# Optimization experiments

Measured on AMD Instinct MI355X. Metric: run time of the kernel, lower is better.

## Reference

```python
import jax, jax.numpy as jnp
import numpy as np

N_HEADS = 16
EMBD = 1024
D_HEAD = EMBD // N_HEADS

def setup_inputs() -> dict:
    key = jax.random.key(0)
    ks = jax.random.split(key, 5)
    x = jax.random.normal(ks[0], (2, 2048, EMBD), dtype=jnp.float32)
    # Linear weights stored torch-style [out, in]; apply as x @ W.T + b
    W_in = jax.random.normal(ks[1], (3 * EMBD, EMBD), dtype=jnp.float32) * (EMBD ** -0.5)
    b_in = jax.random.normal(ks[2], (3 * EMBD,), dtype=jnp.float32) * 0.01
    W_out = jax.random.normal(ks[3], (EMBD, EMBD), dtype=jnp.float32) * (EMBD ** -0.5)
    b_out = jax.random.normal(ks[4], (EMBD,), dtype=jnp.float32) * 0.01
    return {"x": x, "W_in": W_in, "b_in": b_in, "W_out": W_out, "b_out": b_out}

def reference(x, W_in, b_in, W_out, b_out):
    B, S, D = x.shape
    qkv = x @ W_in.T + b_in                      # [B, S, 3D]
    q, k, v = jnp.split(qkv, 3, axis=-1)
    def heads(t):
        return t.reshape(B, S, N_HEADS, D_HEAD).transpose(0, 2, 1, 3)  # [B,H,S,d]
    q, k, v = heads(q), heads(k), heads(v)
    scale = 1.0 / jnp.sqrt(jnp.float32(D_HEAD))
    scores = jnp.einsum('bhqd,bhkd->bhqk', q, k) * scale
    weights = jax.nn.softmax(scores, axis=-1)
    out = jnp.einsum('bhqk,bhkd->bhqd', weights, v)  # [B,H,S,d]
    out = out.transpose(0, 2, 1, 3).reshape(B, S, D)
    return out @ W_out.T + b_out
```

## Files before the change

kernel.cpp:

```cpp
#include <hip/hip_runtime.h>
#include <cstdint>

#define EMBD 1024
#define NH 16
#define DH 64
#define BB 2
#define SS 2048
#define M_TOT (BB*SS)
#define N_QKV (3*EMBD)

typedef __bf16 bf16_t;
typedef bf16_t bf16x8 __attribute__((ext_vector_type(8)));
typedef float f32x4 __attribute__((ext_vector_type(4)));
typedef unsigned short u16;
typedef unsigned int u32;

static __device__ __forceinline__ u16 f2bf(float f) {
    union { float f; unsigned u; } c; c.f = f;
    unsigned u = c.u;
    unsigned r = (u + 0x7FFFu + ((u >> 16) & 1u)) >> 16;
    return (u16)r;
}

#define GLDS16(gp, lp) \
    __builtin_amdgcn_global_load_lds((const __attribute__((address_space(1))) void*)(gp), \
                                     (__attribute__((address_space(3))) void*)(lp), 16, 0, 0)

#define NX8 (M_TOT * EMBD / 8)
#define NWI8 (N_QKV * EMBD / 8)
#define NWO8 (EMBD * EMBD / 8)
__global__ void cast_all(const float* __restrict__ x, const float* __restrict__ wi,
                         const float* __restrict__ wo, u16* __restrict__ xb,
                         u16* __restrict__ wib, u16* __restrict__ wob) {
    int i = blockIdx.x * blockDim.x + threadIdx.x;
    const float* s; u16* d; int off;
    if (i < NX8)              { s = x;  d = xb;  off = i; }
    else if (i < NX8 + NWI8)  { s = wi; d = wib; off = i - NX8; }
    else                      { s = wo; d = wob; off = i - NX8 - NWI8; }
    const float4* s4 = (const float4*)s;
    float4 a = s4[2 * off];
    float4 b = s4[2 * off + 1];
    union { u16 u[8]; uint4 v; } r;
    r.u[0] = f2bf(a.x); r.u[1] = f2bf(a.y); r.u[2] = f2bf(a.z); r.u[3] = f2bf(a.w);
    r.u[4] = f2bf(b.x); r.u[5] = f2bf(b.y); r.u[6] = f2bf(b.z); r.u[7] = f2bf(b.w);
    ((uint4*)d)[off] = r.v;
}

#define QSCALE (0.125f * 1.4426950408889634f)
__global__ __launch_bounds__(256) void gemm_qkv(
    const u16* __restrict__ Xb,
    const u16* __restrict__ Wb,
    const float* __restrict__ b_in,
    u16* __restrict__ Q, u16* __restrict__ Kf, u16* __restrict__ Vpf)
{
    __shared__ u16 AB[3][8192];
    const int t = threadIdx.x;
    const int lane = t & 63;
    const int wave = t >> 6;
    const int wm = wave >> 1, wn = wave & 1;
    const int quad = lane >> 4, l16 = lane & 15;
    const int m0 = blockIdx.y * 128, n0 = blockIdx.x * 128;

    const int s0i = t, s1i = 256 + t;
    const u16* ga0 = Xb + (size_t)(m0 + (s0i >> 2)) * EMBD + (s0i & 3) * 8;
    const u16* ga1 = Xb + (size_t)(m0 + (s1i >> 2)) * EMBD + (s1i & 3) * 8;
    const u16* gb0 = Wb + (size_t)(n0 + (s0i >> 2)) * EMBD + (s0i & 3) * 8;
    const u16* gb1 = Wb + (size_t)(n0 + (s1i >> 2)) * EMBD + (s1i & 3) * 8;

    f32x4 acc[4][4] = {};

#pragma unroll
    for (int p = 0; p < 2; ++p) {
        u16* buf = &AB[p][0];
        GLDS16(ga0 + p * 32, buf + s0i * 8);
        GLDS16(ga1 + p * 32, buf + s1i * 8);
        GLDS16(gb0 + p * 32, buf + 4096 + s0i * 8);
        GLDS16(gb1 + p * 32, buf + 4096 + s1i * 8);
    }

    int bi = 0;
    int bw = 2;
    for (int it = 0; it < EMBD / 32; ++it) {
        asm volatile("s_waitcnt vmcnt(4)" ::: "memory");
        __syncthreads();
        {
            int k0 = (it + 2) * 32;
            u16* buf = &AB[bw][0];
            GLDS16(ga0 + k0, buf + s0i * 8);
            GLDS16(ga1 + k0, buf + s1i * 8);
            GLDS16(gb0 + k0, buf + 4096 + s0i * 8);
            GLDS16(gb1 + k0, buf + 4096 + s1i * 8);
        }
        const u16* As = &AB[bi][0];
        const u16* Bs = &AB[bi][4096];
        bf16x8 af[4], bfr[4];
#pragma unroll
        for (int im = 0; im < 4; ++im)
            af[im] = *(const bf16x8*)(As + (wm * 64 + im * 16 + l16) * 32 + quad * 8);
#pragma unroll
        for (int in = 0; in < 4; ++in)
            bfr[in] = *(const bf16x8*)(Bs + (wn * 64 + in * 16 + l16) * 32 + quad * 8);
#pragma unroll
        for (int im = 0; im < 4; ++im)
#pragma unroll
            for (int in = 0; in < 4; ++in)
                acc[im][in] = __builtin_amdgcn_mfma_f32_16x16x32_bf16(
                    af[im], bfr[in], acc[im][in], 0, 0, 0);
        bi = (bi == 2) ? 0 : bi + 1;
        bw = (bw == 2) ? 0 : bw + 1;
    }

#pragma unroll
    for (int im = 0; im < 4; ++im) {
        int rbase = m0 + wm * 64 + im * 16 + quad * 4;
        int b = rbase >> 11, ss = rbase & (SS - 1);
#pragma unroll
        for (int in = 0; in < 4; ++in) {
            int col = n0 + wn * 64 + in * 16 + l16;
            float bias = b_in[col];
            float v0 = acc[im][in][0] + bias;
            float v1 = acc[im][in][1] + bias;
            float v2 = acc[im][in][2] + bias;
            float v3 = acc[im][in][3] + bias;
            if (col < EMBD) {
                int h = col >> 6, d = col & 63;
                u16* qp = Q + (((size_t)(b * NH + h) * SS) + ss) * DH + d;
                qp[0]      = f2bf(v0 * QSCALE);
                qp[DH]     = f2bf(v1 * QSCALE);
                qp[2 * DH] = f2bf(v2 * QSCALE);
                qp[3 * DH] = f2bf(v3 * QSCALE);
            } else if (col < 2 * EMBD) {
                int c = col - EMBD; int h = c >> 6, d = c & 63;
                int qf = (d >> 3) & 3;
                int sA = (ss >> 1) & 3;
                int sB = (sA + 1) & 3;
                u16* kp = Kf + (size_t)(b * NH + h) * SS * DH
                          + (ss >> 4) * 1024 + (d >> 5) * 512
                          + (ss & 15) * 32 + (d & 7);
                kp[(qf ^ sA) * 8]      = f2bf(v0);
                kp[32 + (qf ^ sA) * 8] = f2bf(v1);
                kp[64 + (qf ^ sB) * 8] = f2bf(v2);
                kp[96 + (qf ^ sB) * 8] = f2bf(v3);
            } else {
                int c = col - 2 * EMBD; int h = c >> 6, d = c & 63;
                int p32 = ((((ss >> 2) & 3) ^ ((d >> 1) & 3)) * 8)
                          + ((ss >> 4) & 1) * 4;
                u32 lo = (u32)f2bf(v0) | ((u32)f2bf(v1) << 16);
                u32 hi = (u32)f2bf(v2) | ((u32)f2bf(v3) << 16);
                uint2 pk; pk.x = lo; pk.y = hi;
                *(uint2*)(Vpf + (size_t)(b * NH + h) * SS * DH
                          + (ss >> 5) * 2048 + (d >> 4) * 512 + (d & 15) * 32 + p32) = pk;
            }
        }
    }
}

#define OST 72
#define NCH (SS / 64)
__global__ __launch_bounds__(256, 2) void attn(
    const u16* __restrict__ Q, const u16* __restrict__ Kf,
    const u16* __restrict__ Vpf, u16* __restrict__ AO)
{
    __shared__ u16 KV[3][8192];
    const int t = threadIdx.x;
    const int lane = t & 63, w = t >> 6;
    const int quad = lane >> 4, l16 = lane & 15;
    const int sq8 = (quad ^ ((l16 >> 1) & 3)) * 8;
    const int b0 = blockIdx.x;
    const int bh = (b0 & 7) * 4 + ((b0 >> 3) & 3);
    const int qt = b0 >> 5;
    const int q0 = qt * 128 + w * 32;

    const u16* Qh = Q + ((size_t)bh * SS + q0) * DH;
    const u16* Kh = Kf + (size_t)bh * SS * DH;
    const u16* Vh = Vpf + (size_t)bh * SS * DH;

    bf16x8 qb[2][2];
#pragma unroll
    for (int qi = 0; qi < 2; ++qi) {
        qb[qi][0] = *(const bf16x8*)(Qh + (qi * 16 + l16) * DH + quad * 8);
        qb[qi][1] = *(const bf16x8*)(Qh + (qi * 16 + l16) * DH + 32 + quad * 8);
    }

    union { u16 u[8]; bf16x8 b; } onesu;
#pragma unroll
    for (int j = 0; j < 8; ++j) onesu.u[j] = 0x3F80u;
    const bf16x8 ones = onesu.b;

    f32x4 o[2][4] = {};
    f32x4 ol[2] = {};

#pragma unroll
    for (int p = 0; p < 2; ++p) {
        GLDS16(Kh + p * 4096 + t * 8,        &KV[p][0] + t * 8);
        GLDS16(Kh + p * 4096 + 2048 + t * 8, &KV[p][0] + 2048 + t * 8);
        GLDS16(Vh + p * 4096 + t * 8,        &KV[p][4096] + t * 8);
        GLDS16(Vh + p * 4096 + 2048 + t * 8, &KV[p][4096] + 2048 + t * 8);
    }

    int bi = 0, bw = 2;
    for (int it = 0; it < NCH; ++it) {
        asm volatile("s_waitcnt vmcnt(4)" ::: "memory");
        __syncthreads();
        if (it < NCH - 1) {
            const u16* kc = Kh + (it + 2) * 4096;
            const u16* vc = Vh + (it + 2) * 4096;
            u16* kb = &KV[bw][0];
            u16* vb = &KV[bw][4096];
            GLDS16(kc + t * 8,        kb + t * 8);
            GLDS16(kc + 2048 + t * 8, kb + 2048 + t * 8);
            GLDS16(vc + t * 8,        vb + t * 8);
            GLDS16(vc + 2048 + t * 8, vb + 2048 + t * 8);
        }
        const u16* Kb = &KV[bi][0];
        const u16* Vb = &KV[bi][4096];
#pragma unroll
        for (int g = 0; g < 2; ++g) {
            bf16x8 ka00 = *(const bf16x8*)(Kb + (2 * g) * 1024 +       l16 * 32 + sq8);
            bf16x8 ka01 = *(const bf16x8*)(Kb + (2 * g) * 1024 + 512 + l16 * 32 + sq8);
            bf16x8 ka10 = *(const bf16x8*)(Kb + (2 * g + 1) * 1024 +       l16 * 32 + sq8);
            bf16x8 ka11 = *(const bf16x8*)(Kb + (2 * g + 1) * 1024 + 512 + l16 * 32 + sq8);
            bf16x8 va0 = *(const bf16x8*)(Vb + g * 2048 +        l16 * 32 + sq8);
            bf16x8 va1 = *(const bf16x8*)(Vb + g * 2048 + 512  + l16 * 32 + sq8);
            bf16x8 va2 = *(const bf16x8*)(Vb + g * 2048 + 1024 + l16 * 32 + sq8);
            bf16x8 va3 = *(const bf16x8*)(Vb + g * 2048 + 1536 + l16 * 32 + sq8);
            bf16x8 pb[2];
#pragma unroll
            for (int qi = 0; qi < 2; ++qi) {
                f32x4 z0 = {0.f, 0.f, 0.f, 0.f};
                f32x4 z1 = {0.f, 0.f, 0.f, 0.f};
                __builtin_amdgcn_s_setprio(1);
                z0 = __builtin_amdgcn_mfma_f32_16x16x32_bf16(ka00, qb[qi][0], z0, 0, 0, 0);
                z0 = __builtin_amdgcn_mfma_f32_16x16x32_bf16(ka01, qb[qi][1], z0, 0, 0, 0);
                z1 = __builtin_amdgcn_mfma_f32_16x16x32_bf16(ka10, qb[qi][0], z1, 0, 0, 0);
                z1 = __builtin_amdgcn_mfma_f32_16x16x32_bf16(ka11, qb[qi][1], z1, 0, 0, 0);
                __builtin_amdgcn_s_setprio(0);
                u32 ue[8];
#pragma unroll
                for (int j = 0; j < 4; ++j) {
                    float e0 = __builtin_amdgcn_exp2f(z0[j]);
                    float e1 = __builtin_amdgcn_exp2f(z1[j]);
                    union { float f; u32 v; } c0, c1;
                    c0.f = e0; c1.f = e1;
                    ue[j] = c0.v + 0x8000u;
                    ue[4 + j] = c1.v + 0x8000u;
                }
                union { uint4 u; bf16x8 b; } cv;
                cv.u.x = __builtin_amdgcn_perm(ue[1], ue[0], 0x07060302u);
                cv.u.y = __builtin_amdgcn_perm(ue[3], ue[2], 0x07060302u);
                cv.u.z = __builtin_amdgcn_perm(ue[5], ue[4], 0x07060302u);
                cv.u.w = __builtin_amdgcn_perm(ue[7], ue[6], 0x07060302u);
                pb[qi] = cv.b;
            }
            __builtin_amdgcn_s_setprio(1);
            o[0][0] = __builtin_amdgcn_mfma_f32_16x16x32_bf16(va0, pb[0], o[0][0], 0, 0, 0);
            o[0][1] = __builtin_amdgcn_mfma_f32_16x16x32_bf16(va1, pb[0], o[0][1], 0, 0, 0);
            o[0][2] = __builtin_amdgcn_mfma_f32_16x16x32_bf16(va2, pb[0], o[0][2], 0, 0, 0);
            o[0][3] = __builtin_amdgcn_mfma_f32_16x16x32_bf16(va3, pb[0], o[0][3], 0, 0, 0);
            ol[0]   = __builtin_amdgcn_mfma_f32_16x16x32_bf16(ones, pb[0], ol[0], 0, 0, 0);
            o[1][0] = __builtin_amdgcn_mfma_f32_16x16x32_bf16(va0, pb[1], o[1][0], 0, 0, 0);
            o[1][1] = __builtin_amdgcn_mfma_f32_16x16x32_bf16(va1, pb[1], o[1][1], 0, 0, 0);
            o[1][2] = __builtin_amdgcn_mfma_f32_16x16x32_bf16(va2, pb[1], o[1][2], 0, 0, 0);
            o[1][3] = __builtin_amdgcn_mfma_f32_16x16x32_bf16(va3, pb[1], o[1][3], 0, 0, 0);
            ol[1]   = __builtin_amdgcn_mfma_f32_16x16x32_bf16(ones, pb[1], ol[1], 0, 0, 0);
            __builtin_amdgcn_s_setprio(0);
        }
        bi = (bi == 2) ? 0 : bi + 1;
        bw = (bw == 2) ? 0 : bw + 1;
    }

    float rl[2];
    rl[0] = 1.0f / ol[0][0];
    rl[1] = 1.0f / ol[1][0];
    __syncthreads();
    u16* Ksc = &KV[0][0];
#pragma unroll
    for (int qi = 0; qi < 2; ++qi)
#pragma unroll
        for (int dt = 0; dt < 4; ++dt)
#pragma unroll
            for (int jj = 0; jj < 2; ++jj) {
                u32 lo_ = (u32)f2bf(o[qi][dt][2 * jj] * rl[qi]);
                u32 hi_ = (u32)f2bf(o[qi][dt][2 * jj + 1] * rl[qi]);
                *(u32*)(Ksc + (w * 32 + qi * 16 + l16) * OST + dt * 16 + quad * 4 + jj * 2) =
                    lo_ | (hi_ << 16);
            }
    __syncthreads();
    const int b = bh >> 4, h = bh & 15;
#pragma unroll
    for (int i = 0; i < 4; ++i) {
        int idx = i * 256 + t;
        int q = idx >> 3, c = idx & 7;
        uint4 vv = *(const uint4*)(Ksc + q * OST + c * 8);
        *(uint4*)(AO + ((size_t)(b * SS + qt * 128 + q)) * EMBD + h * DH + c * 8) = vv;
    }
}

__global__ __launch_bounds__(256) void gemm_out(
    const u16* __restrict__ Ab,
    const u16* __restrict__ Wb,
    const float* __restrict__ b_out,
    float* __restrict__ Out)
{
    __shared__ u16 AB[3][6144];
    const int t = threadIdx.x;
    const int lane = t & 63;
    const int wave = t >> 6;
    const int quad = lane >> 4, l16 = lane & 15;
    const int m0 = blockIdx.y * 128, n0 = blockIdx.x * 64;

    const u16* ga0 = Ab + (size_t)(m0 + (t >> 2)) * EMBD + (t & 3) * 8;
    const u16* ga1 = Ab + (size_t)(m0 + 64 + (t >> 2)) * EMBD + (t & 3) * 8;
    const u16* gb0 = Wb + (size_t)(n0 + (t >> 2)) * EMBD + (t & 3) * 8;

    f32x4 acc[2][4] = {};

#pragma unroll
    for (int p = 0; p < 2; ++p) {
        u16* buf = &AB[p][0];
        GLDS16(ga0 + p * 32, buf + t * 8);
        GLDS16(ga1 + p * 32, buf + 2048 + t * 8);
        GLDS16(gb0 + p * 32, buf + 4096 + t * 8);
    }

    int bi = 0, bw = 2;
    for (int it = 0; it < EMBD / 32; ++it) {
        asm volatile("s_waitcnt vmcnt(3)" ::: "memory");
        __syncthreads();
        {
            int k0 = (it + 2) * 32;
            u16* buf = &AB[bw][0];
            GLDS16(ga0 + k0, buf + t * 8);
            GLDS16(ga1 + k0, buf + 2048 + t * 8);
            GLDS16(gb0 + k0, buf + 4096 + t * 8);
        }
        const u16* As = &AB[bi][0];
        const u16* Bs = &AB[bi][4096];
        bf16x8 af[2], bfr[4];
#pragma unroll
        for (int im = 0; im < 2; ++im)
            af[im] = *(const bf16x8*)(As + (wave * 32 + im * 16 + l16) * 32 + quad * 8);
#pragma unroll
        for (int in = 0; in < 4; ++in)
            bfr[in] = *(const bf16x8*)(Bs + (in * 16 + l16) * 32 + quad * 8);
#pragma unroll
        for (int im = 0; im < 2; ++im)
#pragma unroll
            for (int in = 0; in < 4; ++in)
                acc[im][in] = __builtin_amdgcn_mfma_f32_16x16x32_bf16(
                    af[im], bfr[in], acc[im][in], 0, 0, 0);
        bi = (bi == 2) ? 0 : bi + 1;
        bw = (bw == 2) ? 0 : bw + 1;
    }

#pragma unroll
    for (int im = 0; im < 2; ++im) {
        int rbase = m0 + wave * 32 + im * 16 + quad * 4;
#pragma unroll
        for (int in = 0; in < 4; ++in) {
            int col = n0 + in * 16 + l16;
            float bias = b_out[col];
#pragma unroll
            for (int j = 0; j < 4; ++j)
                Out[(size_t)(rbase + j) * EMBD + col] = acc[im][in][j] + bias;
        }
    }
}

extern "C" void kernel_launch(void* const* d_in, const int* in_sizes, int n_in,
                              void* d_out, int out_size, void* d_ws, size_t ws_size,
                              hipStream_t stream)
{
    (void)in_sizes; (void)n_in; (void)out_size; (void)ws_size;
    const float* x     = (const float*)d_in[0];
    const float* W_in  = (const float*)d_in[1];
    const float* b_in  = (const float*)d_in[2];
    const float* W_out = (const float*)d_in[3];
    const float* b_out = (const float*)d_in[4];
    float* out = (float*)d_out;

    char* ws = (char*)d_ws;
    u16* xb  = (u16*)(ws);
    u16* wib = (u16*)(ws + 8u  * 1024 * 1024);
    u16* wob = (u16*)(ws + 14u * 1024 * 1024);
    u16* Qw  = (u16*)(ws + 16u * 1024 * 1024);
    u16* Kw  = (u16*)(ws + 24u * 1024 * 1024);
    u16* Vpw = (u16*)(ws + 32u * 1024 * 1024);
    u16* AO  = (u16*)(ws + 40u * 1024 * 1024);

    cast_all<<<(NX8 + NWI8 + NWO8) / 256, 256, 0, stream>>>(x, W_in, W_out, xb, wib, wob);
    gemm_qkv<<<dim3(N_QKV / 128, M_TOT / 128), 256, 0, stream>>>(xb, wib, b_in, Qw, Kw, Vpw);
    attn<<<512, 256, 0, stream>>>(Qw, Kw, Vpw, AO);
    gemm_out<<<dim3(EMBD / 64, M_TOT / 128), 256, 0, stream>>>(AO, wob, b_out, out);
}
```

Before: 176.9 us.

## Stage Q/K epilogue through LDS for 16-byte stores and remap blocks per XCD

The QKV GEMM epilogue for Q and K tiles now writes bf16 results into shared memory first and then emits 16-byte vectorized global stores, in place of scattered 2-byte stores. K's swizzled layout is reproduced at 8-element granularity. The grid is flattened to 1D and block IDs are remapped so consecutive blocks on the same XCD share M rows, which is meant to improve L2 reuse. The cost is extra LDS traffic and two barriers in the epilogue.

```diff
diff --git a/kernel.cpp b/kernel.cpp
--- a/kernel.cpp
+++ b/kernel.cpp
@@ -59,7 +59,9 @@
     const int wave = t >> 6;
     const int wm = wave >> 1, wn = wave & 1;
     const int quad = lane >> 4, l16 = lane & 15;
-    const int m0 = blockIdx.y * 128, n0 = blockIdx.x * 128;
+    const int wg = blockIdx.x;
+    const int sw = (wg & 7) * 96 + (wg >> 3);
+    const int m0 = (sw / 24) * 128, n0 = (sw % 24) * 128;
 
     const int s0i = t, s1i = 256 + t;
     const u16* ga0 = Xb + (size_t)(m0 + (s0i >> 2)) * EMBD + (s0i & 3) * 8;
@@ -110,38 +112,62 @@
         bw = (bw == 2) ? 0 : bw + 1;
     }
 
-#pragma unroll
-    for (int im = 0; im < 4; ++im) {
-        int rbase = m0 + wm * 64 + im * 16 + quad * 4;
-        int b = rbase >> 11, ss = rbase & (SS - 1);
-#pragma unroll
-        for (int in = 0; in < 4; ++in) {
-            int col = n0 + wn * 64 + in * 16 + l16;
-            float bias = b_in[col];
-            float v0 = acc[im][in][0] + bias;
-            float v1 = acc[im][in][1] + bias;
-            float v2 = acc[im][in][2] + bias;
-            float v3 = acc[im][in][3] + bias;
-            if (col < EMBD) {
-                int h = col >> 6, d = col & 63;
-                u16* qp = Q + (((size_t)(b * NH + h) * SS) + ss) * DH + d;
-                qp[0]      = f2bf(v0 * QSCALE);
-                qp[DH]     = f2bf(v1 * QSCALE);
-                qp[2 * DH] = f2bf(v2 * QSCALE);
-                qp[3 * DH] = f2bf(v3 * QSCALE);
-            } else if (col < 2 * EMBD) {
-                int c = col - EMBD; int h = c >> 6, d = c & 63;
-                int qf = (d >> 3) & 3;
-                int sA = (ss >> 1) & 3;
-                int sB = (sA + 1) & 3;
+    if (n0 < 2 * EMBD) {
+        asm volatile("s_waitcnt vmcnt(0)" ::: "memory");
+        __syncthreads();
+        u16* S = &AB[0][0];
+        const bool isQ = (n0 < EMBD);
+        const float scl = isQ ? QSCALE : 1.0f;
+#pragma unroll
+        for (int im = 0; im < 4; ++im) {
+            int rl = wm * 64 + im * 16 + quad * 4;
+#pragma unroll
+            for (int in = 0; in < 4; ++in) {
+                int cl = wn * 64 + in * 16 + l16;
+                float bias = b_in[n0 + cl];
+#pragma unroll
+                for (int j = 0; j < 4; ++j)
+                    S[(rl + j) * 136 + cl] = f2bf((acc[im][in][j] + bias) * scl);
+            }
+        }
+        __syncthreads();
+        if (isQ) {
+#pragma unroll
+            for (int i = 0; i < 8; ++i) {
+                int unit = i * 256 + t;
+                int row = unit >> 4, cu = unit & 15;
+                uint4 v = *(const uint4*)(S + row * 136 + cu * 8);
+                int m = m0 + row; int b = m >> 11, ss = m & (SS - 1);
+                int col = n0 + cu * 8; int h = col >> 6, d = col & 63;
+                *(uint4*)(Q + (((size_t)(b * NH + h) * SS) + ss) * DH + d) = v;
+            }
+        } else {
+#pragma unroll
+            for (int i = 0; i < 8; ++i) {
+                int unit = i * 256 + t;
+                int row = unit >> 4, cu = unit & 15;
+                uint4 v = *(const uint4*)(S + row * 136 + cu * 8);
+                int m = m0 + row; int b = m >> 11, ss = m & (SS - 1);
+                int c = (n0 - EMBD) + cu * 8; int h = c >> 6, db = c & 63;
                 u16* kp = Kf + (size_t)(b * NH + h) * SS * DH
-                          + (ss >> 4) * 1024 + (d >> 5) * 512
-                          + (ss & 15) * 32 + (d & 7);
-                kp[(qf ^ sA) * 8]      = f2bf(v0);
-                kp[32 + (qf ^ sA) * 8] = f2bf(v1);
-                kp[64 + (qf ^ sB) * 8] = f2bf(v2);
-                kp[96 + (qf ^ sB) * 8] = f2bf(v3);
-            } else {
+                          + (ss >> 4) * 1024 + (db >> 5) * 512 + (ss & 15) * 32
+                          + (((db >> 3) & 3) ^ ((ss >> 1) & 3)) * 8;
+                *(uint4*)kp = v;
+            }
+        }
+    } else {
+#pragma unroll
+        for (int im = 0; im < 4; ++im) {
+            int rbase = m0 + wm * 64 + im * 16 + quad * 4;
+            int b = rbase >> 11, ss = rbase & (SS - 1);
+#pragma unroll
+            for (int in = 0; in < 4; ++in) {
+                int col = n0 + wn * 64 + in * 16 + l16;
+                float bias = b_in[col];
+                float v0 = acc[im][in][0] + bias;
+                float v1 = acc[im][in][1] + bias;
+                float v2 = acc[im][in][2] + bias;
+                float v3 = acc[im][in][3] + bias;
                 int c = col - 2 * EMBD; int h = c >> 6, d = c & 63;
                 int p32 = ((((ss >> 2) & 3) ^ ((d >> 1) & 3)) * 8)
                           + ((ss >> 4) & 1) * 4;
@@ -389,7 +415,7 @@
     u16* AO  = (u16*)(ws + 40u * 1024 * 1024);
 
     cast_all<<<(NX8 + NWI8 + NWO8) / 256, 256, 0, stream>>>(x, W_in, W_out, xb, wib, wob);
-    gemm_qkv<<<dim3(N_QKV / 128, M_TOT / 128), 256, 0, stream>>>(xb, wib, b_in, Qw, Kw, Vpw);
+    gemm_qkv<<<768, 256, 0, stream>>>(xb, wib, b_in, Qw, Kw, Vpw);
     attn<<<512, 256, 0, stream>>>(Qw, Kw, Vpw, AO);
     gemm_out<<<dim3(EMBD / 64, M_TOT / 128), 256, 0, stream>>>(AO, wob, b_out, out);
 }
```

Measured after the change: 182.6 us. 1.03x slower.
